# Kernel tuning notes

Measured on AMD Instinct MI355X. Metric: run time of the kernel, lower is better.

## Reference

```python
import jax, jax.numpy as jnp
import numpy as np

B, S, C_IN, C_OUT = 8, 2048, 512, 512

def setup_inputs() -> dict:
    key = jax.random.key(0)
    k1, k2, k3, k4 = jax.random.split(key, 4)
    sc = 1.0 / np.sqrt(C_IN)
    return {
        "x": jax.random.normal(k1, (B, S, C_IN), dtype=jnp.float32),
        "Wq": jax.random.normal(k2, (C_OUT, C_IN), dtype=jnp.float32) * sc,
        "Wk": jax.random.normal(k3, (C_OUT, C_IN), dtype=jnp.float32) * sc,
        "Wv": jax.random.normal(k4, (C_OUT, C_IN), dtype=jnp.float32) * sc,
    }

def reference(x, Wq, Wk, Wv):
    # x: [B,S,Cin]; weights [Cout,Cin] (torch Linear convention, no bias)
    C = Wq.shape[0]
    dk = jnp.sqrt(jnp.float32(1.0) / C)  # torch: sqrt(1/out_features)
    q = jnp.einsum('bsi,oi->bso', x, Wq)
    k = jnp.einsum('bsi,oi->bso', x, Wk)
    v = jnp.einsum('bsi,oi->bso', x, Wv)
    phi_q = jax.nn.elu(q * dk) + 1.0
    phi_k = jax.nn.elu(k * dk) + 1.0
    b = x.shape[0]
    mem0 = jnp.zeros((b, C, C), x.dtype)   # running sum of phi_k v^T
    zeta0 = jnp.zeros((b, C), x.dtype)     # running sum of phi_k
    def step(carry, inp):
        mem, zeta = carry
        pq, pk, vv = inp                    # each [B,C]
        dm = pk[:, :, None] * vv[:, None, :]              # [B,C,C]
        scale = jnp.einsum('bc,bc->b', pq, pk + zeta) + 1e-5
        num = jnp.einsum('bc,bcd->bd', pq, dm + mem)
        y = num / scale[:, None]
        # state updates are under torch.no_grad -> detach
        new_mem = jax.lax.stop_gradient(mem + dm)
        new_zeta = jax.lax.stop_gradient(zeta + pk)
        return (new_mem, new_zeta), y
    xs = (phi_q.transpose(1, 0, 2), phi_k.transpose(1, 0, 2), v.transpose(1, 0, 2))
    _, ys = jax.lax.scan(step, (mem0, zeta0), xs)  # ys: [S,B,C]
    return ys.transpose(1, 0, 2)                   # [B,S,C]
```

## Files before the change

### kernel.cpp

```cpp
#include <hip/hip_runtime.h>


constexpr int Bn  = 8;
constexpr int Sn  = 2048;
constexpr int Cn  = 512;
constexpr int Tn  = 128;
constexpr int NCn = 16;
constexpr float DKf = 0.04419417382415922f;

typedef __attribute__((ext_vector_type(8))) short bf16x8;
typedef __attribute__((ext_vector_type(4))) float f32x4;

__device__ __forceinline__ unsigned short f2bf(float f) {
  unsigned u = __float_as_uint(f);
  u = (u + 0x7fffu + ((u >> 16) & 1u)) >> 16;
  return (unsigned short)u;
}
__device__ __forceinline__ float bf2f(unsigned short h) {
  return __uint_as_float(((unsigned)h) << 16);
}
__device__ __forceinline__ float phi_f(float u) {
  float s = u * DKf;
  return s > 0.0f ? s + 1.0f : __expf(s);
}

__device__ __forceinline__ void stage128x32(const unsigned short* __restrict__ g,
                                            int ld, unsigned short* lds,
                                            int wid, int lane) {
#pragma unroll
  for (int cc = 0; cc < 2; ++cc) {
    const int row = cc * 64 + wid * 16 + (lane >> 2);
    const int ks  = (lane & 3) ^ ((row >> 1) & 3);
    const unsigned short* src = g + (size_t)row * ld + ks * 8;
    unsigned short* dst = lds + (size_t)(cc * 256 + wid * 64) * 8;
    __builtin_amdgcn_global_load_lds(
        (const __attribute__((address_space(1))) void*)src,
        (__attribute__((address_space(3))) void*)dst, 16, 0, 0);
  }
}

__device__ __forceinline__ void mm_loop(const unsigned short* __restrict__ Ag, int lda,
                                        const unsigned short* __restrict__ Bg, int ldb,
                                        int nkt,
                                        unsigned short* Al, unsigned short* Bl,
                                        f32x4 acc[4][4]) {
  const int t = threadIdx.x, wid = t >> 6, lane = t & 63;
  const int wm = wid >> 1, wn = wid & 1;
  const int fr = lane & 15, kb = lane >> 4;
  stage128x32(Ag, lda, Al, wid, lane);
  stage128x32(Bg, ldb, Bl, wid, lane);
  __syncthreads();
  int cur = 0;
  for (int kt = 0; kt < nkt; ++kt) {
    const int nxt = cur ^ 1;
    if (kt + 1 < nkt) {
      stage128x32(Ag + (kt + 1) * 32, lda, Al + nxt * 4096, wid, lane);
      stage128x32(Bg + (kt + 1) * 32, ldb, Bl + nxt * 4096, wid, lane);
    }
    const unsigned short* Ac = Al + cur * 4096;
    const unsigned short* Bc = Bl + cur * 4096;
    bf16x8 af[4], bf[4];
#pragma unroll
    for (int m = 0; m < 4; ++m) {
      const int r = wm * 64 + m * 16 + fr;
      af[m] = *(const bf16x8*)&Ac[r * 32 + ((kb ^ ((r >> 1) & 3)) << 3)];
    }
#pragma unroll
    for (int n = 0; n < 4; ++n) {
      const int r = wn * 64 + n * 16 + fr;
      bf[n] = *(const bf16x8*)&Bc[r * 32 + ((kb ^ ((r >> 1) & 3)) << 3)];
    }
#pragma unroll
    for (int m = 0; m < 4; ++m)
#pragma unroll
      for (int n = 0; n < 4; ++n)
        acc[m][n] = __builtin_amdgcn_mfma_f32_16x16x32_bf16(af[m], bf[n], acc[m][n], 0, 0, 0);
    __syncthreads();
    cur = nxt;
  }
}

__global__ __launch_bounds__(256) void k_cast_x(const float* __restrict__ x,
                                                unsigned short* __restrict__ xb) {
  const size_t i8 = ((size_t)blockIdx.x * 256 + threadIdx.x) * 8;
  float4 a = *(const float4*)&x[i8];
  float4 b = *(const float4*)&x[i8 + 4];
  uint4 o;
  o.x = (unsigned)f2bf(a.x) | ((unsigned)f2bf(a.y) << 16);
  o.y = (unsigned)f2bf(a.z) | ((unsigned)f2bf(a.w) << 16);
  o.z = (unsigned)f2bf(b.x) | ((unsigned)f2bf(b.y) << 16);
  o.w = (unsigned)f2bf(b.z) | ((unsigned)f2bf(b.w) << 16);
  *(uint4*)&xb[i8] = o;
}

__global__ __launch_bounds__(256) void k_cast_w(const float* __restrict__ Wq,
                                                const float* __restrict__ Wk,
                                                const float* __restrict__ Wv,
                                                unsigned short* __restrict__ Wb) {
  const int z = blockIdx.y;
  const float* __restrict__ src = (z == 0) ? Wq : (z == 1 ? Wk : Wv);
  const size_t i8 = ((size_t)blockIdx.x * 256 + threadIdx.x) * 8;
  float4 a = *(const float4*)&src[i8];
  float4 b = *(const float4*)&src[i8 + 4];
  uint4 o;
  o.x = (unsigned)f2bf(a.x) | ((unsigned)f2bf(a.y) << 16);
  o.y = (unsigned)f2bf(a.z) | ((unsigned)f2bf(a.w) << 16);
  o.z = (unsigned)f2bf(b.x) | ((unsigned)f2bf(b.y) << 16);
  o.w = (unsigned)f2bf(b.z) | ((unsigned)f2bf(b.w) << 16);
  *(uint4*)&Wb[(size_t)z * Cn * Cn + i8] = o;
}

__global__ __launch_bounds__(256) void k_proj(
    const unsigned short* __restrict__ xb, const unsigned short* __restrict__ Wb,
    unsigned short* __restrict__ PQ, unsigned short* __restrict__ PK,
    unsigned short* __restrict__ PKt, unsigned short* __restrict__ Vt,
    float* __restrict__ zsum)
{
  __shared__ unsigned short Al[2 * 128 * 32], Bl[2 * 128 * 32];
  __shared__ float zbuf[2][128];
  const int bid = blockIdx.x;
  const int xcd = bid & 7, idx = bid >> 3;
  const int n = idx & 3, z = (idx >> 2) % 3, mloc = idx / 12;
  const int n0 = n * 128, m0 = (xcd * 16 + mloc) * 128;
  const int t = threadIdx.x, wid = t >> 6, lane = t & 63;
  const int wm = wid >> 1, wn = wid & 1;
  f32x4 acc[4][4];
  const f32x4 zero = {0.f, 0.f, 0.f, 0.f};
#pragma unroll
  for (int m = 0; m < 4; ++m)
#pragma unroll
    for (int nn = 0; nn < 4; ++nn) acc[m][nn] = zero;

  mm_loop(xb + (size_t)m0 * Cn, Cn,
          Wb + (size_t)z * Cn * Cn + (size_t)n0 * Cn, Cn, Cn / 32, Al, Bl, acc);

  float ps[4] = {0.f, 0.f, 0.f, 0.f};
#pragma unroll
  for (int m = 0; m < 4; ++m)
#pragma unroll
    for (int nn = 0; nn < 4; ++nn) {
      const int row0 = m0 + wm * 64 + m * 16 + ((lane >> 4) << 2);
      const int col  = n0 + wn * 64 + nn * 16 + (lane & 15);
      f32x4 v = acc[m][nn];
      if (z == 0) {
#pragma unroll
        for (int j = 0; j < 4; ++j)
          PQ[(size_t)(row0 + j) * Cn + col] = f2bf(phi_f(v[j]));
      } else if (z == 1) {
        ushort4 p;
#pragma unroll
        for (int j = 0; j < 4; ++j) {
          unsigned short u = f2bf(phi_f(v[j]));
          PK[(size_t)(row0 + j) * Cn + col] = u;
          (&p.x)[j] = u;
          ps[nn] += bf2f(u);
        }
        const int b = row0 >> 11, tq = row0 & (Sn - 1);
        *(ushort4*)&PKt[((size_t)b * Cn + col) * Sn + tq] = p;
      } else {
        ushort4 p;
#pragma unroll
        for (int j = 0; j < 4; ++j) (&p.x)[j] = f2bf(v[j]);
        const int b = row0 >> 11, tq = row0 & (Sn - 1);
        *(ushort4*)&Vt[((size_t)b * Cn + col) * Sn + tq] = p;
      }
    }

  if (z == 1) {
#pragma unroll
    for (int nn = 0; nn < 4; ++nn) {
      float v = ps[nn];
      v += __shfl_xor(v, 16); v += __shfl_xor(v, 32);
      if (lane < 16) zbuf[wm][wn * 64 + nn * 16 + lane] = v;
    }
    __syncthreads();
    if (t < 128) {
      const int b = m0 >> 11, ch = (m0 >> 7) & 15;
      zsum[((size_t)b * NCn + ch) * Cn + n0 + t] = zbuf[0][t] + zbuf[1][t];
    }
  }
}

__global__ __launch_bounds__(256) void k_gram(
    const unsigned short* __restrict__ PQ, const unsigned short* __restrict__ PK,
    unsigned short* __restrict__ Abuf, float* __restrict__ scale)
{
  __shared__ unsigned short Al[2 * 128 * 32], Bl[2 * 128 * 32];
  __shared__ float rsmem[2][128];
  const int b = blockIdx.y, ch = blockIdx.x;
  const size_t base = ((size_t)b * Sn + ch * Tn) * Cn;
  f32x4 acc[4][4];
  const f32x4 zero = {0.f, 0.f, 0.f, 0.f};
#pragma unroll
  for (int m = 0; m < 4; ++m)
#pragma unroll
    for (int n = 0; n < 4; ++n) acc[m][n] = zero;

  mm_loop(PQ + base, Cn, PK + base, Cn, Cn / 32, Al, Bl, acc);

  const int t = threadIdx.x, wid = t >> 6, lane = t & 63;
  const int wm = wid >> 1, wn = wid & 1;
  float rsum[4][4];
#pragma unroll
  for (int m = 0; m < 4; ++m)
#pragma unroll
    for (int j = 0; j < 4; ++j) rsum[m][j] = 0.f;
#pragma unroll
  for (int m = 0; m < 4; ++m)
#pragma unroll
    for (int n = 0; n < 4; ++n) {
      f32x4 v = acc[m][n];
#pragma unroll
      for (int j = 0; j < 4; ++j) {
        const int row = wm * 64 + m * 16 + ((lane >> 4) << 2) + j;
        const int col = wn * 64 + n * 16 + (lane & 15);
        unsigned short u = (col <= row) ? f2bf(v[j]) : 0;
        Abuf[((size_t)(b * NCn + ch) * Tn + row) * Tn + col] = u;
        rsum[m][j] += bf2f(u);
      }
    }
#pragma unroll
  for (int m = 0; m < 4; ++m)
#pragma unroll
    for (int j = 0; j < 4; ++j) {
      float r = rsum[m][j];
      r += __shfl_xor(r, 1); r += __shfl_xor(r, 2);
      r += __shfl_xor(r, 4); r += __shfl_xor(r, 8);
      if ((lane & 15) == 0)
        rsmem[wn][wm * 64 + m * 16 + ((lane >> 4) << 2) + j] = r;
    }
  __syncthreads();
  if (t < 128)
    scale[(size_t)b * Sn + ch * Tn + t] = rsmem[0][t] + rsmem[1][t];
}

__global__ __launch_bounds__(512) void k_zpre(const float* __restrict__ zsum,
                                              float* __restrict__ zpre) {
  const int b = blockIdx.x, c = threadIdx.x;
  float run = 0.f;
  for (int ch = 0; ch < NCn; ++ch) {
    zpre[((size_t)b * NCn + ch) * Cn + c] = run;
    run += zsum[((size_t)b * NCn + ch) * Cn + c];
  }
}

__global__ __launch_bounds__(256) void k_scale(const unsigned short* __restrict__ PQ,
                                               const float* __restrict__ zpre,
                                               float* __restrict__ scale) {
  const int b = blockIdx.y;
  const int w = threadIdx.x >> 6, lane = threadIdx.x & 63;
  const int row = blockIdx.x * 4 + w;
  const int ch = row >> 7;
  const unsigned short* pq = PQ + ((size_t)b * Sn + row) * Cn + lane * 8;
  const float* zp = zpre + ((size_t)b * NCn + ch) * Cn + lane * 8;
  uint4 q = *(const uint4*)pq;
  float4 z0 = *(const float4*)zp, z1 = *(const float4*)(zp + 4);
  float d = bf2f((unsigned short)(q.x & 0xffff)) * z0.x
          + bf2f((unsigned short)(q.x >> 16))    * z0.y
          + bf2f((unsigned short)(q.y & 0xffff)) * z0.z
          + bf2f((unsigned short)(q.y >> 16))    * z0.w
          + bf2f((unsigned short)(q.z & 0xffff)) * z1.x
          + bf2f((unsigned short)(q.z >> 16))    * z1.y
          + bf2f((unsigned short)(q.w & 0xffff)) * z1.z
          + bf2f((unsigned short)(q.w >> 16))    * z1.w;
#pragma unroll
  for (int off = 32; off > 0; off >>= 1) d += __shfl_xor(d, off);
  if (lane == 0) scale[(size_t)b * Sn + row] += d + 1e-5f;
}

__device__ __forceinline__ void stage64x128(const unsigned short* __restrict__ g,
                                            int ld, unsigned short* lds,
                                            int wid, int lane) {
#pragma unroll
  for (int i = 0; i < 4; ++i) {
    const int row = wid * 16 + i * 4 + (lane >> 4);
    const int s   = (lane & 15) ^ (row & 7);
    const unsigned short* src = g + (size_t)row * ld + s * 8;
    unsigned short* dst = lds + (size_t)(wid * 16 + i * 4) * 128;
    __builtin_amdgcn_global_load_lds(
        (const __attribute__((address_space(1))) void*)src,
        (__attribute__((address_space(3))) void*)dst, 16, 0, 0);
  }
}

__global__ __launch_bounds__(256) void k_kvp(
    const unsigned short* __restrict__ PKt, const unsigned short* __restrict__ Vt,
    unsigned short* __restrict__ Mpre)
{
  __shared__ unsigned short Al[2 * 64 * 128], Bl[2 * 64 * 128];
  const int bid = blockIdx.x;
  const int b = bid & 7, idx = bid >> 3;
  const int d0 = (idx & 7) * 64, c0 = (idx >> 3) * 64;
  const int t = threadIdx.x, wid = t >> 6, lane = t & 63;
  const int wm = wid >> 1, wn = wid & 1;
  const int fr = lane & 15, kb = lane >> 4;
  f32x4 acc[2][2];
  const f32x4 zero = {0.f, 0.f, 0.f, 0.f};
#pragma unroll
  for (int m = 0; m < 2; ++m)
#pragma unroll
    for (int n = 0; n < 2; ++n) acc[m][n] = zero;
  const unsigned short* Ag = PKt + ((size_t)b * Cn + c0) * Sn;
  const unsigned short* Bg = Vt  + ((size_t)b * Cn + d0) * Sn;
  stage64x128(Ag, Sn, Al, wid, lane);
  stage64x128(Bg, Sn, Bl, wid, lane);
  __syncthreads();
  int cur = 0;
  for (int ch = 0; ch < NCn; ++ch) {
    const int nxt = cur ^ 1;
    if (ch + 1 < NCn) {
      stage64x128(Ag + (ch + 1) * Tn, Sn, Al + nxt * 8192, wid, lane);
      stage64x128(Bg + (ch + 1) * Tn, Sn, Bl + nxt * 8192, wid, lane);
    }
    if (ch > 0) {
#pragma unroll
      for (int m = 0; m < 2; ++m)
#pragma unroll
        for (int n = 0; n < 2; ++n) {
          const int c_row = c0 + wm * 32 + m * 16 + (kb << 2);
          const int d     = d0 + wn * 32 + n * 16 + fr;
          ushort4 p;
#pragma unroll
          for (int j = 0; j < 4; ++j) (&p.x)[j] = f2bf(acc[m][n][j]);
          *(ushort4*)&Mpre[((size_t)(b * NCn + ch) * Cn + d) * Cn + c_row] = p;
        }
    }
    const unsigned short* Ac = Al + cur * 8192;
    const unsigned short* Bc = Bl + cur * 8192;
#pragma unroll
    for (int kt = 0; kt < 4; ++kt) {
      bf16x8 af[2], bf[2];
#pragma unroll
      for (int m = 0; m < 2; ++m) {
        const int r = wm * 32 + m * 16 + fr;
        af[m] = *(const bf16x8*)&Ac[r * 128 + (((kt * 4 + kb) ^ (r & 7)) << 3)];
      }
#pragma unroll
      for (int n = 0; n < 2; ++n) {
        const int r = wn * 32 + n * 16 + fr;
        bf[n] = *(const bf16x8*)&Bc[r * 128 + (((kt * 4 + kb) ^ (r & 7)) << 3)];
      }
#pragma unroll
      for (int m = 0; m < 2; ++m)
#pragma unroll
        for (int n = 0; n < 2; ++n)
          acc[m][n] = __builtin_amdgcn_mfma_f32_16x16x32_bf16(af[m], bf[n], acc[m][n], 0, 0, 0);
    }
    __syncthreads();
    cur = nxt;
  }
}

__global__ __launch_bounds__(256) void k_avinter(
    const unsigned short* __restrict__ Abuf, const unsigned short* __restrict__ Vt,
    const unsigned short* __restrict__ PQ, const unsigned short* __restrict__ Mpre,
    const float* __restrict__ scale, float* __restrict__ out)
{
  __shared__ unsigned short Al[2 * 128 * 32], Bl[2 * 128 * 32];
  const int bid = blockIdx.x;
  const int logical = (bid & 7) * 64 + (bid >> 3);
  const int d0 = (logical & 3) * 128;
  const int ch = (logical >> 2) & 15;
  const int b  = logical >> 6;
  const int t0 = ch * Tn;
  f32x4 acc[4][4];
  const f32x4 zero = {0.f, 0.f, 0.f, 0.f};
#pragma unroll
  for (int m = 0; m < 4; ++m)
#pragma unroll
    for (int n = 0; n < 4; ++n) acc[m][n] = zero;

  mm_loop(Abuf + (size_t)(b * NCn + ch) * Tn * Tn, Tn,
          Vt + ((size_t)b * Cn + d0) * Sn + t0, Sn, Tn / 32, Al, Bl, acc);
  if (ch > 0)
    mm_loop(PQ + ((size_t)b * Sn + t0) * Cn, Cn,
            Mpre + ((size_t)(b * NCn + ch) * Cn + d0) * Cn, Cn, Cn / 32, Al, Bl, acc);

  const int t = threadIdx.x, wid = t >> 6, lane = t & 63;
  const int wm = wid >> 1, wn = wid & 1;
#pragma unroll
  for (int m = 0; m < 4; ++m)
#pragma unroll
    for (int n = 0; n < 4; ++n) {
      const int row0 = t0 + wm * 64 + m * 16 + ((lane >> 4) << 2);
      const int col  = d0 + wn * 64 + n * 16 + (lane & 15);
      f32x4 v = acc[m][n];
#pragma unroll
      for (int j = 0; j < 4; ++j) {
        const size_t sidx = (size_t)b * Sn + row0 + j;
        out[sidx * Cn + col] = v[j] / scale[sidx];
      }
    }
}

extern "C" void kernel_launch(void* const* d_in, const int* in_sizes, int n_in,
                              void* d_out, int out_size, void* d_ws, size_t ws_size,
                              hipStream_t stream)
{
  const float* x  = (const float*)d_in[0];
  const float* Wq = (const float*)d_in[1];
  const float* Wk = (const float*)d_in[2];
  const float* Wv = (const float*)d_in[3];
  float* out = (float*)d_out;

  unsigned short* xb   = (unsigned short*)d_ws;
  unsigned short* Wb   = xb   + (size_t)Bn * Sn * Cn;
  unsigned short* PQ   = Wb   + (size_t)3 * Cn * Cn;
  unsigned short* PK   = PQ   + (size_t)Bn * Sn * Cn;
  unsigned short* PKt  = PK   + (size_t)Bn * Sn * Cn;
  unsigned short* Vt   = PKt  + (size_t)Bn * Sn * Cn;
  unsigned short* Abuf = Vt   + (size_t)Bn * Sn * Cn;
  unsigned short* Mpre = Abuf + (size_t)Bn * NCn * Tn * Tn;
  float* scale = (float*)(Mpre + (size_t)Bn * NCn * Cn * Cn);
  float* zsum  = scale + (size_t)Bn * Sn;
  float* zpre  = zsum  + (size_t)Bn * NCn * Cn;
  (void)ws_size; (void)in_sizes; (void)n_in; (void)out_size;

  hipLaunchKernelGGL(k_cast_x, dim3(4096), dim3(256), 0, stream, x, xb);
  hipLaunchKernelGGL(k_cast_w, dim3(128, 3), dim3(256), 0, stream, Wq, Wk, Wv, Wb);
  hipLaunchKernelGGL(k_proj, dim3(1536), dim3(256), 0, stream, xb, Wb, PQ, PK, PKt, Vt, zsum);
  hipLaunchKernelGGL(k_zpre, dim3(Bn), dim3(512), 0, stream, zsum, zpre);
  hipLaunchKernelGGL(k_gram, dim3(NCn, Bn), dim3(256), 0, stream, PQ, PK, Abuf, scale);
  hipLaunchKernelGGL(k_scale, dim3(Sn / 4, Bn), dim3(256), 0, stream, PQ, zpre, scale);
  hipLaunchKernelGGL(k_kvp, dim3(512), dim3(256), 0, stream, PKt, Vt, Mpre);
  hipLaunchKernelGGL(k_avinter, dim3(512), dim3(256), 0, stream, Abuf, Vt, PQ, Mpre, scale, out);
}
```

Before: 138.6 us.

## Fuse zeta prefix and scale into k_gram; pipeline staging with partial vmcnt waits

Removes the k_zpre and k_scale launches. Each k_gram block now computes the zeta prefix for its chunk from zsum into LDS and adds the inter-chunk scale term directly. Separately, the double-buffered loops in mm_loop and k_kvp replace __syncthreads with explicit partial s_waitcnt vmcnt plus s_barrier, so the next tile's async LDS loads can stay in flight while the current tile is computed. The intent is to cut launch overhead and stalls on outstanding global loads, at the cost of relying on exact vmcnt counts matching the number of staging instructions.

Measured after the change: 133.9 us. 3.4% less time.

```diff
diff --git a/kernel.cpp b/kernel.cpp
--- a/kernel.cpp
+++ b/kernel.cpp
@@ -49,14 +49,18 @@
   const int fr = lane & 15, kb = lane >> 4;
   stage128x32(Ag, lda, Al, wid, lane);
   stage128x32(Bg, ldb, Bl, wid, lane);
-  __syncthreads();
   int cur = 0;
   for (int kt = 0; kt < nkt; ++kt) {
     const int nxt = cur ^ 1;
     if (kt + 1 < nkt) {
       stage128x32(Ag + (kt + 1) * 32, lda, Al + nxt * 4096, wid, lane);
       stage128x32(Bg + (kt + 1) * 32, ldb, Bl + nxt * 4096, wid, lane);
-    }
+      asm volatile("s_waitcnt vmcnt(4)" ::: "memory");
+    } else {
+      asm volatile("s_waitcnt vmcnt(0)" ::: "memory");
+    }
+    __builtin_amdgcn_s_barrier();
+    asm volatile("" ::: "memory");
     const unsigned short* Ac = Al + cur * 4096;
     const unsigned short* Bc = Bl + cur * 4096;
     bf16x8 af[4], bf[4];
@@ -75,7 +79,8 @@
 #pragma unroll
       for (int n = 0; n < 4; ++n)
         acc[m][n] = __builtin_amdgcn_mfma_f32_16x16x32_bf16(af[m], bf[n], acc[m][n], 0, 0, 0);
-    __syncthreads();
+    __builtin_amdgcn_s_barrier();
+    asm volatile("" ::: "memory");
     cur = nxt;
   }
 }
@@ -183,10 +188,12 @@
 
 __global__ __launch_bounds__(256) void k_gram(
     const unsigned short* __restrict__ PQ, const unsigned short* __restrict__ PK,
+    const float* __restrict__ zsum,
     unsigned short* __restrict__ Abuf, float* __restrict__ scale)
 {
   __shared__ unsigned short Al[2 * 128 * 32], Bl[2 * 128 * 32];
   __shared__ float rsmem[2][128];
+  __shared__ float zpl[512];
   const int b = blockIdx.y, ch = blockIdx.x;
   const size_t base = ((size_t)b * Sn + ch * Tn) * Cn;
   f32x4 acc[4][4];
@@ -229,43 +236,33 @@
       if ((lane & 15) == 0)
         rsmem[wn][wm * 64 + m * 16 + ((lane >> 4) << 2) + j] = r;
     }
+#pragma unroll
+  for (int e = 0; e < 2; ++e) {
+    const int c = t + e * 256;
+    float s = 0.f;
+    for (int ch2 = 0; ch2 < ch; ++ch2)
+      s += zsum[((size_t)b * NCn + ch2) * Cn + c];
+    zpl[c] = s;
+  }
   __syncthreads();
-  if (t < 128)
-    scale[(size_t)b * Sn + ch * Tn + t] = rsmem[0][t] + rsmem[1][t];
-}
-
-__global__ __launch_bounds__(512) void k_zpre(const float* __restrict__ zsum,
-                                              float* __restrict__ zpre) {
-  const int b = blockIdx.x, c = threadIdx.x;
-  float run = 0.f;
-  for (int ch = 0; ch < NCn; ++ch) {
-    zpre[((size_t)b * NCn + ch) * Cn + c] = run;
-    run += zsum[((size_t)b * NCn + ch) * Cn + c];
-  }
-}
-
-__global__ __launch_bounds__(256) void k_scale(const unsigned short* __restrict__ PQ,
-                                               const float* __restrict__ zpre,
-                                               float* __restrict__ scale) {
-  const int b = blockIdx.y;
-  const int w = threadIdx.x >> 6, lane = threadIdx.x & 63;
-  const int row = blockIdx.x * 4 + w;
-  const int ch = row >> 7;
-  const unsigned short* pq = PQ + ((size_t)b * Sn + row) * Cn + lane * 8;
-  const float* zp = zpre + ((size_t)b * NCn + ch) * Cn + lane * 8;
-  uint4 q = *(const uint4*)pq;
-  float4 z0 = *(const float4*)zp, z1 = *(const float4*)(zp + 4);
-  float d = bf2f((unsigned short)(q.x & 0xffff)) * z0.x
-          + bf2f((unsigned short)(q.x >> 16))    * z0.y
-          + bf2f((unsigned short)(q.y & 0xffff)) * z0.z
-          + bf2f((unsigned short)(q.y >> 16))    * z0.w
-          + bf2f((unsigned short)(q.z & 0xffff)) * z1.x
-          + bf2f((unsigned short)(q.z >> 16))    * z1.y
-          + bf2f((unsigned short)(q.w & 0xffff)) * z1.z
-          + bf2f((unsigned short)(q.w >> 16))    * z1.w;
-#pragma unroll
-  for (int off = 32; off > 0; off >>= 1) d += __shfl_xor(d, off);
-  if (lane == 0) scale[(size_t)b * Sn + row] += d + 1e-5f;
+  const int row = t >> 1, half = (t & 1) * 256;
+  const unsigned short* pq = PQ + base + (size_t)row * Cn + half;
+  float dacc = 0.f;
+  for (int i = 0; i < 256; i += 8) {
+    uint4 q = *(const uint4*)(pq + i);
+    dacc += bf2f((unsigned short)(q.x & 0xffff)) * zpl[half + i + 0]
+          + bf2f((unsigned short)(q.x >> 16))    * zpl[half + i + 1]
+          + bf2f((unsigned short)(q.y & 0xffff)) * zpl[half + i + 2]
+          + bf2f((unsigned short)(q.y >> 16))    * zpl[half + i + 3]
+          + bf2f((unsigned short)(q.z & 0xffff)) * zpl[half + i + 4]
+          + bf2f((unsigned short)(q.z >> 16))    * zpl[half + i + 5]
+          + bf2f((unsigned short)(q.w & 0xffff)) * zpl[half + i + 6]
+          + bf2f((unsigned short)(q.w >> 16))    * zpl[half + i + 7];
+  }
+  dacc += __shfl_xor(dacc, 1);
+  if ((t & 1) == 0)
+    scale[(size_t)b * Sn + ch * Tn + row] =
+        rsmem[0][row] + rsmem[1][row] + dacc + 1e-5f;
 }
 
 __device__ __forceinline__ void stage64x128(const unsigned short* __restrict__ g,
@@ -304,14 +301,18 @@
   const unsigned short* Bg = Vt  + ((size_t)b * Cn + d0) * Sn;
   stage64x128(Ag, Sn, Al, wid, lane);
   stage64x128(Bg, Sn, Bl, wid, lane);
-  __syncthreads();
   int cur = 0;
   for (int ch = 0; ch < NCn; ++ch) {
     const int nxt = cur ^ 1;
     if (ch + 1 < NCn) {
       stage64x128(Ag + (ch + 1) * Tn, Sn, Al + nxt * 8192, wid, lane);
       stage64x128(Bg + (ch + 1) * Tn, Sn, Bl + nxt * 8192, wid, lane);
-    }
+      asm volatile("s_waitcnt vmcnt(8)" ::: "memory");
+    } else {
+      asm volatile("s_waitcnt vmcnt(0)" ::: "memory");
+    }
+    __builtin_amdgcn_s_barrier();
+    asm volatile("" ::: "memory");
     if (ch > 0) {
 #pragma unroll
       for (int m = 0; m < 2; ++m)
@@ -346,7 +347,8 @@
         for (int n = 0; n < 2; ++n)
           acc[m][n] = __builtin_amdgcn_mfma_f32_16x16x32_bf16(af[m], bf[n], acc[m][n], 0, 0, 0);
     }
-    __syncthreads();
+    __builtin_amdgcn_s_barrier();
+    asm volatile("" ::: "memory");
     cur = nxt;
   }
 }
@@ -413,15 +415,12 @@
   unsigned short* Mpre = Abuf + (size_t)Bn * NCn * Tn * Tn;
   float* scale = (float*)(Mpre + (size_t)Bn * NCn * Cn * Cn);
   float* zsum  = scale + (size_t)Bn * Sn;
-  float* zpre  = zsum  + (size_t)Bn * NCn * Cn;
   (void)ws_size; (void)in_sizes; (void)n_in; (void)out_size;
 
   hipLaunchKernelGGL(k_cast_x, dim3(4096), dim3(256), 0, stream, x, xb);
   hipLaunchKernelGGL(k_cast_w, dim3(128, 3), dim3(256), 0, stream, Wq, Wk, Wv, Wb);
   hipLaunchKernelGGL(k_proj, dim3(1536), dim3(256), 0, stream, xb, Wb, PQ, PK, PKt, Vt, zsum);
-  hipLaunchKernelGGL(k_zpre, dim3(Bn), dim3(512), 0, stream, zsum, zpre);
-  hipLaunchKernelGGL(k_gram, dim3(NCn, Bn), dim3(256), 0, stream, PQ, PK, Abuf, scale);
-  hipLaunchKernelGGL(k_scale, dim3(Sn / 4, Bn), dim3(256), 0, stream, PQ, zpre, scale);
+  hipLaunchKernelGGL(k_gram, dim3(NCn, Bn), dim3(256), 0, stream, PQ, PK, zsum, Abuf, scale);
   hipLaunchKernelGGL(k_kvp, dim3(512), dim3(256), 0, stream, PKt, Vt, Mpre);
   hipLaunchKernelGGL(k_avinter, dim3(512), dim3(256), 0, stream, Abuf, Vt, PQ, Mpre, scale, out);
 }
```
